# Optimization experiments

Measured on AMD Instinct MI355X. Metric: run time of the kernel, lower is better.

The kernel has to match this reference:

```python
import jax, jax.numpy as jnp
import numpy as np

B, N, D = 4, 1024, 1024
H, DH = 16, 64            # heads, dim_head; inner_dim = H*DH = D
CTX_N, CTX_D = 77, 768    # CLIP text context
FF_IN, FF_HID = 8 * D, 4 * D  # GEGLU: proj to 2*4*D, gate to 4*D
EPS = 1e-5
SCALE = DH ** -0.5
NL = 256                  # 2**8 levels for all quantizers
ZP_QKV = 128.0            # asymmetric 8-bit zero point for q/k/v
ZP_W = 0.0                # always_zero=True for softmax-weight quantizer


def _round_ste(t):
    return t + jax.lax.stop_gradient(jnp.round(t) - t)


def _fake_quant(x, delta, zp):
    xq = jnp.clip(_round_ste(x / delta) + zp, 0.0, NL - 1.0)
    return (xq - zp) * delta


def _ln(x, w, b):
    m = x.mean(-1, keepdims=True)
    v = x.var(-1, keepdims=True)
    return (x - m) * jax.lax.rsqrt(v + EPS) * w + b


def _split_heads(t):  # [b, n, h*d] -> [b, h, n, d]
    b, n, _ = t.shape
    return t.reshape(b, n, H, DH).transpose(0, 2, 1, 3)


def _attn(x, ctx, wq, wk, wv, wo, bo, dq, dk, dv, dw):
    q = _split_heads(x @ wq)
    k = _split_heads(ctx @ wk)
    v = _split_heads(ctx @ wv)
    qq = _fake_quant(q, dq, ZP_QKV)
    kk = _fake_quant(k, dk, ZP_QKV)
    sim = jnp.einsum('bhid,bhjd->bhij', qq, kk) * SCALE
    attn = jax.nn.softmax(sim, axis=-1)
    aw = _fake_quant(attn, dw, ZP_W)
    vv = _fake_quant(v, dv, ZP_QKV)
    out = jnp.einsum('bhij,bhjd->bhid', aw, vv)
    b, _, n, _ = out.shape
    out = out.transpose(0, 2, 1, 3).reshape(b, n, H * DH)
    return out @ wo + bo


def _geglu_ff(x, w1, b1, w2, b2):
    h = x @ w1 + b1
    a, g = jnp.split(h, 2, axis=-1)
    return (a * jax.nn.gelu(g, approximate=False)) @ w2 + b2


def setup_inputs() -> dict:
    key = jax.random.key(0)
    ks = jax.random.split(key, 16)
    w = lambda i, shp, s: jax.random.normal(ks[i], shp, jnp.float32) * s
    sD = D ** -0.5
    sC = CTX_D ** -0.5
    return {
        'x': jax.random.normal(ks[0], (B, N, D), jnp.float32),
        'context': jax.random.normal(ks[1], (B, CTX_N, CTX_D), jnp.float32),
        'norm1_w': jnp.ones((D,), jnp.float32), 'norm1_b': jnp.zeros((D,), jnp.float32),
        'norm2_w': jnp.ones((D,), jnp.float32), 'norm2_b': jnp.zeros((D,), jnp.float32),
        'norm3_w': jnp.ones((D,), jnp.float32), 'norm3_b': jnp.zeros((D,), jnp.float32),
        'a1_wq': w(2, (D, D), sD), 'a1_wk': w(3, (D, D), sD), 'a1_wv': w(4, (D, D), sD),
        'a1_wo': w(5, (D, D), sD), 'a1_bo': jnp.zeros((D,), jnp.float32),
        'a2_wq': w(6, (D, D), sD), 'a2_wk': w(7, (CTX_D, D), sC), 'a2_wv': w(8, (CTX_D, D), sC),
        'a2_wo': w(9, (D, D), sD), 'a2_bo': jnp.zeros((D,), jnp.float32),
        'ff_w1': w(10, (D, FF_IN), sD), 'ff_b1': jnp.zeros((FF_IN,), jnp.float32),
        'ff_w2': w(11, (FF_HID, D), FF_HID ** -0.5), 'ff_b2': jnp.zeros((D,), jnp.float32),
        'd1_q': jnp.asarray(0.02, jnp.float32), 'd1_k': jnp.asarray(0.02, jnp.float32),
        'd1_v': jnp.asarray(0.02, jnp.float32), 'd1_w': jnp.asarray(1.0 / 255.0, jnp.float32),
        'd2_q': jnp.asarray(0.02, jnp.float32), 'd2_k': jnp.asarray(0.02, jnp.float32),
        'd2_v': jnp.asarray(0.02, jnp.float32), 'd2_w': jnp.asarray(1.0 / 255.0, jnp.float32),
    }


def reference(x, context, norm1_w, norm1_b, norm2_w, norm2_b, norm3_w, norm3_b,
              a1_wq, a1_wk, a1_wv, a1_wo, a1_bo,
              a2_wq, a2_wk, a2_wv, a2_wo, a2_bo,
              ff_w1, ff_b1, ff_w2, ff_b2,
              d1_q, d1_k, d1_v, d1_w, d2_q, d2_k, d2_v, d2_w):
    # attn1: quantized self-attention
    x = _attn(_ln(x, norm1_w, norm1_b), _ln(x, norm1_w, norm1_b),
              a1_wq, a1_wk, a1_wv, a1_wo, a1_bo, d1_q, d1_k, d1_v, d1_w) + x
    # attn2: quantized cross-attention with text context
    x = _attn(_ln(x, norm2_w, norm2_b), context,
              a2_wq, a2_wk, a2_wv, a2_wo, a2_bo, d2_q, d2_k, d2_v, d2_w) + x
    # GEGLU feed-forward
    x = _geglu_ff(_ln(x, norm3_w, norm3_b), ff_w1, ff_b1, ff_w2, ff_b2) + x
    return x
```

## Files before the change

kernel.cpp:

```cpp
#include <hip/hip_runtime.h>
#include <math.h>


typedef unsigned short u16;
typedef __attribute__((ext_vector_type(8))) short short8;
typedef __attribute__((ext_vector_type(4))) float f32x4;

__device__ inline float b2f(u16 v) { return __uint_as_float(((unsigned)v) << 16); }
__device__ inline u16 f2b(float f) {
  unsigned u = __float_as_uint(f);
  unsigned r = u + 0x7fffu + ((u >> 16) & 1u);
  return (u16)(r >> 16);
}

__device__ inline float exp2_fast(float x) {
#if __has_builtin(__builtin_amdgcn_exp2f)
  return __builtin_amdgcn_exp2f(x);
#else
  return __expf(x * 0.6931471805599453f);
#endif
}

__device__ inline void glds16(const u16* g, u16* l) {
  __builtin_amdgcn_global_load_lds(
      (const __attribute__((address_space(1))) void*)g,
      (__attribute__((address_space(3))) void*)l, 16, 0, 0);
}

__global__ __launch_bounds__(256) void transpose_k(const float* __restrict__ in,
                                                   u16* __restrict__ out,
                                                   int R, int C) {
  __shared__ float t[32][33];
  int tx = threadIdx.x & 31, ty = threadIdx.x >> 5;
  int c0 = blockIdx.x * 32, r0 = blockIdx.y * 32;
#pragma unroll
  for (int i = 0; i < 32; i += 8)
    t[ty + i][tx] = in[(size_t)(r0 + ty + i) * C + c0 + tx];
  __syncthreads();
#pragma unroll
  for (int i = 0; i < 32; i += 8)
    out[(size_t)(c0 + ty + i) * R + r0 + tx] = f2b(t[tx][ty + i]);
}

struct TrBatch { const float* in[4]; u16* out[4]; int R[4]; };
__global__ __launch_bounds__(256) void transpose4_k(TrBatch a) {
  int z = blockIdx.z;
  const float* in = a.in[z];
  u16* out = a.out[z];
  int R = a.R[z];
  int r0 = blockIdx.y * 32;
  if (r0 >= R) return;
  __shared__ float t[32][33];
  int tx = threadIdx.x & 31, ty = threadIdx.x >> 5;
  int c0 = blockIdx.x * 32;
#pragma unroll
  for (int i = 0; i < 32; i += 8)
    t[ty + i][tx] = in[(size_t)(r0 + ty + i) * 1024 + c0 + tx];
  __syncthreads();
#pragma unroll
  for (int i = 0; i < 32; i += 8)
    out[(size_t)(c0 + ty + i) * R + r0 + tx] = f2b(t[tx][ty + i]);
}

__global__ __launch_bounds__(256) void tr16_k(const u16* __restrict__ in,
                                              u16* __restrict__ out, int NK,
                                              int NKP) {
  __shared__ u16 t[32][33];
  int tx = threadIdx.x & 31, ty = threadIdx.x >> 5;
  int n0 = blockIdx.x * 32, c0 = blockIdx.y * 32, b = blockIdx.z;
  const u16* ib = in + (size_t)b * NK * 1024;
  u16* ob = out + (size_t)b * 1024 * NKP;
#pragma unroll
  for (int i = 0; i < 32; i += 8) {
    int n = n0 + ty + i;
    n = n < NK ? n : NK - 1;
    t[ty + i][tx] = ib[(size_t)n * 1024 + c0 + tx];
  }
  __syncthreads();
#pragma unroll
  for (int i = 0; i < 32; i += 8)
    ob[(size_t)(c0 + ty + i) * NKP + n0 + tx] = t[tx][ty + i];
}

__global__ __launch_bounds__(256) void cast_k(const float* __restrict__ in,
                                              u16* __restrict__ out) {
  int i = (blockIdx.x * 256 + threadIdx.x) * 4;
  float4 v = *(const float4*)(in + i);
  out[i + 0] = f2b(v.x);
  out[i + 1] = f2b(v.y);
  out[i + 2] = f2b(v.z);
  out[i + 3] = f2b(v.w);
}

__global__ __launch_bounds__(256) void ln_k(const float* __restrict__ X,
                                            const float* __restrict__ W,
                                            const float* __restrict__ Bi,
                                            u16* __restrict__ Out) {
  const int row = blockIdx.x, tid = threadIdx.x;
  float4 x = *(const float4*)(X + (size_t)row * 1024 + tid * 4);
  float s = x.x + x.y + x.z + x.w;
  float s2 = x.x * x.x + x.y * x.y + x.z * x.z + x.w * x.w;
#pragma unroll
  for (int off = 32; off >= 1; off >>= 1) {
    s += __shfl_down(s, off);
    s2 += __shfl_down(s2, off);
  }
  __shared__ float red[8];
  int wave = tid >> 6, lane = tid & 63;
  if (lane == 0) { red[wave] = s; red[4 + wave] = s2; }
  __syncthreads();
  s = red[0] + red[1] + red[2] + red[3];
  s2 = red[4] + red[5] + red[6] + red[7];
  float mean = s * 0.0009765625f;
  float var = s2 * 0.0009765625f - mean * mean;
  float rs = rsqrtf(var + 1e-5f);
  float4 w = *(const float4*)(W + tid * 4);
  float4 b = *(const float4*)(Bi + tid * 4);
  u16* orow = Out + (size_t)row * 1024 + tid * 4;
  orow[0] = f2b((x.x - mean) * rs * w.x + b.x);
  orow[1] = f2b((x.y - mean) * rs * w.y + b.y);
  orow[2] = f2b((x.z - mean) * rs * w.z + b.z);
  orow[3] = f2b((x.w - mean) * rs * w.w + b.w);
}

template <int EPI, int TM>
__global__ __launch_bounds__(256, 2) void gemm_bt(
    const u16* __restrict__ A, int lda, const u16* __restrict__ Bt, int ldb,
    void* __restrict__ Cp, int ldc, const float* __restrict__ bias,
    const float* __restrict__ res, int ldr, const float* __restrict__ dp,
    const float* __restrict__ dp2, const float* __restrict__ dp3,
    size_t segsz, int M, int N, int K) {
  __shared__ __align__(16) u16 As[TM * 64];
  __shared__ __align__(16) u16 Bs[128 * 64];
  const int tid = threadIdx.x;
  const int lane = tid & 63, wave = tid >> 6;
  const int qd = lane >> 4, cl = lane & 15;
  const int wm = (wave & 1) * (TM / 2), wn = (wave >> 1) << 6;
  const int m0 = blockIdx.x * TM, n0 = blockIdx.y * 128;

  f32x4 acc[TM / 32][4];
  const f32x4 zero = {0.f, 0.f, 0.f, 0.f};
#pragma unroll
  for (int i = 0; i < TM / 32; i++)
#pragma unroll
    for (int j = 0; j < 4; j++) acc[i][j] = zero;

  for (int k0 = 0; k0 < K; k0 += 64) {
    __syncthreads();
#pragma unroll
    for (int it = 0; it < TM / 32; ++it) {
      int ch = it * 256 + tid;
      int r = ch >> 3, cc = (ch & 7) << 3;
      int gr = m0 + r;
      gr = gr < M ? gr : M - 1;
      glds16(A + (size_t)gr * lda + k0 + cc, As + ch * 8);
    }
#pragma unroll
    for (int it = 0; it < 4; ++it) {
      int ch = it * 256 + tid;
      int r = ch >> 3, cc = (ch & 7) << 3;
      glds16(Bt + (size_t)(n0 + r) * ldb + k0 + cc, Bs + ch * 8);
    }
    __syncthreads();
#pragma unroll
    for (int ks = 0; ks < 64; ks += 32) {
      short8 af[TM / 32], bf[4];
#pragma unroll
      for (int t = 0; t < TM / 32; t++)
        af[t] = *(const short8*)(As + (wm + t * 16 + cl) * 64 + ks + qd * 8);
#pragma unroll
      for (int t = 0; t < 4; t++)
        bf[t] = *(const short8*)(Bs + (wn + t * 16 + cl) * 64 + ks + qd * 8);
#pragma unroll
      for (int mt = 0; mt < TM / 32; mt++)
#pragma unroll
        for (int nt = 0; nt < 4; nt++)
          acc[mt][nt] = __builtin_amdgcn_mfma_f32_16x16x32_bf16(
              af[mt], bf[nt], acc[mt][nt], 0, 0, 0);
    }
  }

  float dscale = 1.f;
  u16* qbase = (u16*)Cp;
  if constexpr (EPI == 0) dscale = 1.0f / dp[0];
  if constexpr (EPI == 2) {
    int seg = n0 >> 10;
    const float* ds = (seg == 0) ? dp : ((seg == 1) ? dp2 : dp3);
    dscale = 1.0f / ds[0];
    qbase = (u16*)Cp + (size_t)seg * segsz;
  }
#pragma unroll
  for (int mt = 0; mt < TM / 32; ++mt) {
#pragma unroll
    for (int r = 0; r < 4; ++r) {
      int row = m0 + wm + mt * 16 + qd * 4 + r;
      if (row >= M) continue;
#pragma unroll
      for (int nt = 0; nt < 4; ++nt) {
        int col = n0 + wn + nt * 16 + cl;
        float v = acc[mt][nt][r];
        if constexpr (EPI == 0) {
          float xq = rintf(v * dscale) + 128.f;
          xq = fminf(fmaxf(xq, 0.f), 255.f);
          qbase[(size_t)row * ldc + col] = f2b(xq - 128.f);
        } else if constexpr (EPI == 2) {
          float xq = rintf(v * dscale) + 128.f;
          xq = fminf(fmaxf(xq, 0.f), 255.f);
          qbase[(size_t)row * ldc + (col & 1023)] = f2b(xq - 128.f);
        } else {
          v += bias[col] + res[(size_t)row * ldr + col];
          ((float*)Cp)[(size_t)row * ldc + col] = v;
        }
      }
    }
  }
}

#define VMW(n) asm volatile("s_waitcnt vmcnt(" #n ")" ::: "memory")
#define LGKM0() asm volatile("s_waitcnt lgkmcnt(0)" ::: "memory")
#define SBAR() __builtin_amdgcn_s_barrier()
#define SCHED0() __builtin_amdgcn_sched_barrier(0)

#define ST_A(P, MH, K0)                                                      \
  do {                                                                       \
    _Pragma("unroll") for (int it = 0; it < 2; ++it) {                       \
      int r_ = (MH) * 128 + it * 64 + sr;                                    \
      glds16(Ag + (size_t)(m0 + r_) * 1024 + (K0) + ((sc ^ (r_ & 7)) << 3),  \
             As + (P) * 16384 + r_ * 64 + (sc << 3));                        \
    }                                                                        \
  } while (0)

#define ST_B(P, BH, K0)                                                      \
  do {                                                                       \
    _Pragma("unroll") for (int it = 0; it < 2; ++it) {                       \
      int r_ = it * 64 + sr;                                                 \
      glds16(W1t + (size_t)((BH) * 4096 + n0 + r_) * 1024 + (K0) +           \
                 ((sc ^ (r_ & 7)) << 3),                                     \
             Bs + (P) * 16384 + ((BH) * 128 + r_) * 64 + (sc << 3));         \
    }                                                                        \
  } while (0)

#define RDA(P, MH)                                                           \
  do {                                                                       \
    _Pragma("unroll") for (int mf = 0; mf < 4; ++mf) {                       \
      int row_ = (MH) * 128 + wr * 64 + mf * 16 + cl;                        \
      _Pragma("unroll") for (int ks = 0; ks < 2; ++ks)                       \
        af[mf * 2 + ks] = *(const short8*)(As + (P) * 16384 + row_ * 64 +    \
                                           (((ks * 4 + qd) ^ (cl & 7)) << 3)); \
    }                                                                        \
  } while (0)

#define RDB(P, NH, DST)                                                      \
  do {                                                                       \
    _Pragma("unroll") for (int nf = 0; nf < 2; ++nf) {                       \
      int j_ = (NH) * 128 + wc * 32 + nf * 16 + cl;                          \
      _Pragma("unroll") for (int ks = 0; ks < 2; ++ks)                       \
        DST[nf * 2 + ks] = *(const short8*)(Bs + (P) * 16384 + j_ * 64 +     \
                                            (((ks * 4 + qd) ^ (cl & 7)) << 3)); \
    }                                                                        \
  } while (0)

#define MFMAQ(MH, NH, BSET)                                                  \
  do {                                                                       \
    _Pragma("unroll") for (int mf = 0; mf < 4; ++mf)                         \
      _Pragma("unroll") for (int nf = 0; nf < 2; ++nf)                       \
        _Pragma("unroll") for (int ks = 0; ks < 2; ++ks)                     \
          acc[(MH) * 4 + mf][(NH) * 2 + nf] =                                \
              __builtin_amdgcn_mfma_f32_16x16x32_bf16(                       \
                  af[mf * 2 + ks], BSET[nf * 2 + ks],                        \
                  acc[(MH) * 4 + mf][(NH) * 2 + nf], 0, 0, 0);               \
  } while (0)

#define KTILE(P, KN, LAST)                                                   \
  do {                                                                       \
                            \
    RDA(P, 0);                                                               \
    RDB(P, 0, bU);                                                           \
    if (!(LAST)) ST_A((P) ^ 1, 0, KN);                                       \
    SBAR();                                                                  \
    LGKM0();                                                                 \
    SCHED0();                                                                \
    __builtin_amdgcn_s_setprio(1);                                           \
    MFMAQ(0, 0, bU);                                                         \
    __builtin_amdgcn_s_setprio(0);                                           \
    SCHED0();                                                                \
    if (LAST) { VMW(0); } else { VMW(2); }                                   \
    SBAR();                                                                  \
                                    \
    RDB(P, 1, bV);                                                           \
    if (!(LAST)) ST_B((P) ^ 1, 0, KN);                                       \
    SBAR();                                                                  \
    LGKM0();                                                                 \
    SCHED0();                                                                \
    __builtin_amdgcn_s_setprio(1);                                           \
    MFMAQ(0, 1, bV);                                                         \
    __builtin_amdgcn_s_setprio(0);                                           \
    SCHED0();                                                                \
    SBAR();                                                                  \
                                    \
    RDA(P, 1);                                                               \
    if (!(LAST)) ST_A((P) ^ 1, 1, KN);                                       \
    SBAR();                                                                  \
    LGKM0();                                                                 \
    SCHED0();                                                                \
    __builtin_amdgcn_s_setprio(1);                                           \
    MFMAQ(1, 1, bV);                                                         \
    __builtin_amdgcn_s_setprio(0);                                           \
    SCHED0();                                                                \
    SBAR();                                                                  \
                                       \
    if (!(LAST)) ST_B((P) ^ 1, 1, KN);                                       \
    SBAR();                                                                  \
    LGKM0();                                                                 \
    SCHED0();                                                                \
    __builtin_amdgcn_s_setprio(1);                                           \
    MFMAQ(1, 0, bU);                                                         \
    __builtin_amdgcn_s_setprio(0);                                           \
    SCHED0();                                                                \
    if (!(LAST)) VMW(4);                                                     \
    SBAR();                                                                  \
  } while (0)

__global__ __launch_bounds__(512, 1) void ff1_geglu8_k(
    const u16* __restrict__ Ag, const u16* __restrict__ W1t,
    const float* __restrict__ b1, u16* __restrict__ gg) {
  __shared__ __align__(16) u16 smem[65536];
  u16* As = smem;
  u16* Bs = smem + 32768;
  const int tid = threadIdx.x;
  const int lane = tid & 63, wave = tid >> 6;
  const int qd = lane >> 4, cl = lane & 15;
  const int wr = wave >> 2, wc = wave & 3;
  const int m0 = blockIdx.x * 256;
  const int n0 = blockIdx.y * 128;
  const int sr = tid >> 3, sc = tid & 7;

  f32x4 acc[8][4];
  const f32x4 zero = {0.f, 0.f, 0.f, 0.f};
#pragma unroll
  for (int i = 0; i < 8; ++i)
#pragma unroll
    for (int j = 0; j < 4; ++j) acc[i][j] = zero;
  short8 af[8], bU[4], bV[4];

  ST_A(0, 0, 0);
  ST_B(0, 0, 0);
  ST_A(0, 1, 0);
  ST_B(0, 1, 0);
  VMW(0);
  SBAR();
  SCHED0();

  int p = 0;
#pragma unroll 1
  for (int t = 0; t < 15; ++t) {
    KTILE(p, (t + 1) * 64, 0);
    p ^= 1;
  }
  KTILE(1, 0, 1);

#pragma unroll
  for (int i = 0; i < 8; ++i) {
    const int row = m0 + (i >> 2) * 128 + wr * 64 + (i & 3) * 16 + qd * 4;
#pragma unroll
    for (int nf = 0; nf < 2; ++nf) {
      const int col = n0 + wc * 32 + nf * 16 + cl;
      const float ba = b1[col];
      const float bg = b1[4096 + col];
#pragma unroll
      for (int r = 0; r < 4; ++r) {
        float a = acc[i][nf][r] + ba;
        float g = acc[i][2 + nf][r] + bg;
        float ge = 0.5f * g * (1.0f + erff(g * 0.70710678118654752f));
        gg[(size_t)(row + r) * 4096 + col] = f2b(a * ge);
      }
    }
  }
}

__global__ __launch_bounds__(256, 4) void attn_k(
    const u16* __restrict__ Q, const u16* __restrict__ Kb,
    const u16* __restrict__ VbT, u16* __restrict__ O,
    const float* dqp, const float* dkp, const float* dvp, const float* dwp,
    int NK, int NKP) {
  __shared__ __align__(16) u16 Ks[64 * 64];
  __shared__ __align__(16) u16 VTs[64 * 64];
  __shared__ __align__(16) u16 Ps[4][16 * 72];
  const int tid = threadIdx.x;
  const int lane = tid & 63, wave = tid >> 6;
  const int qd = lane >> 4, cl = lane & 15;
  const int b = blockIdx.z, h = blockIdx.y, qt = blockIdx.x;
  const float ss2 = dqp[0] * dkp[0] * 0.125f * 1.4426950408889634f;
  const float oscale = dwp[0] * dvp[0];
  const float inv_dw = 1.0f / dwp[0];
  const f32x4 zero = {0.f, 0.f, 0.f, 0.f};

  short8 qf0, qf1;
  {
    const u16* qrow =
        Q + (size_t)(b * 1024 + qt * 64 + wave * 16 + cl) * 1024 + h * 64;
    qf0 = *(const short8*)(qrow + qd * 8);
    qf1 = *(const short8*)(qrow + 32 + qd * 8);
  }

  const u16* kbase = Kb + (size_t)(b * NK) * 1024 + h * 64;
  const u16* vtbase = VbT + ((size_t)b * 1024 + h * 64) * NKP;
  const int r_st = tid >> 3;
  const int c_sw = (((tid & 7) ^ (r_st & 7)) << 3);

  float m_s = -1e30f, l_s = 0.f;
  for (int j0 = 0; j0 < NK; j0 += 64) {
    __syncthreads();
#pragma unroll
    for (int it = 0; it < 2; ++it) {
      int j = j0 + it * 32 + r_st;
      j = j < NK ? j : NK - 1;
      glds16(kbase + (size_t)j * 1024 + c_sw, Ks + (it * 256 + tid) * 8);
    }
    __syncthreads();
    const bool full = (j0 + 64 <= NK);
    float sc[16];
#pragma unroll
    for (int nt = 0; nt < 4; ++nt) {
      const int row = nt * 16 + cl, sw = cl & 7;
      short8 kf0 = *(const short8*)(Ks + row * 64 + ((qd ^ sw) << 3));
      short8 kf1 = *(const short8*)(Ks + row * 64 + (((4 | qd) ^ sw) << 3));
      f32x4 st = zero;
      st = __builtin_amdgcn_mfma_f32_16x16x32_bf16(kf0, qf0, st, 0, 0, 0);
      st = __builtin_amdgcn_mfma_f32_16x16x32_bf16(kf1, qf1, st, 0, 0, 0);
#pragma unroll
      for (int r = 0; r < 4; ++r) {
        int key = j0 + nt * 16 + qd * 4 + r;
        sc[nt * 4 + r] = (full || key < NK) ? st[r] * ss2 : -1e30f;
      }
    }
    float t0 = fmaxf(fmaxf(sc[0], sc[1]), sc[2]);
    float t1 = fmaxf(fmaxf(sc[3], sc[4]), sc[5]);
    float t2 = fmaxf(fmaxf(sc[6], sc[7]), sc[8]);
    float t3 = fmaxf(fmaxf(sc[9], sc[10]), sc[11]);
    float t4 = fmaxf(fmaxf(sc[12], sc[13]), sc[14]);
    float mx = fmaxf(fmaxf(fmaxf(t0, t1), fmaxf(t2, t3)), fmaxf(t4, sc[15]));
    mx = fmaxf(mx, __shfl_xor(mx, 16));
    mx = fmaxf(mx, __shfl_xor(mx, 32));
    float mn = fmaxf(m_s, mx);
    float ss = 0.f;
#pragma unroll
    for (int i = 0; i < 16; ++i) ss += exp2_fast(sc[i] - mn);
    ss += __shfl_xor(ss, 16);
    ss += __shfl_xor(ss, 32);
    l_s = l_s * exp2_fast(m_s - mn) + ss;
    m_s = mn;
  }
  const float mb = m_s + log2f(l_s) - log2f(inv_dw);

  f32x4 oacc[4];
#pragma unroll
  for (int t = 0; t < 4; t++) oacc[t] = zero;

  for (int j0 = 0; j0 < NK; j0 += 64) {
    __syncthreads();
#pragma unroll
    for (int it = 0; it < 2; ++it) {
      int r = it * 32 + r_st;
      int j = j0 + r;
      j = j < NK ? j : NK - 1;
      glds16(kbase + (size_t)j * 1024 + c_sw, Ks + (it * 256 + tid) * 8);
      glds16(vtbase + (size_t)r * NKP + j0 + c_sw, VTs + (it * 256 + tid) * 8);
    }
    __syncthreads();
    const bool full = (j0 + 64 <= NK);
#pragma unroll
    for (int nt = 0; nt < 4; ++nt) {
      const int row = nt * 16 + cl, sw = cl & 7;
      short8 kf0 = *(const short8*)(Ks + row * 64 + ((qd ^ sw) << 3));
      short8 kf1 = *(const short8*)(Ks + row * 64 + (((4 | qd) ^ sw) << 3));
      f32x4 st = zero;
      st = __builtin_amdgcn_mfma_f32_16x16x32_bf16(kf0, qf0, st, 0, 0, 0);
      st = __builtin_amdgcn_mfma_f32_16x16x32_bf16(kf1, qf1, st, 0, 0, 0);
      unsigned a[4];
#pragma unroll
      for (int r = 0; r < 4; ++r) {
        int key = j0 + nt * 16 + qd * 4 + r;
        float aw = 0.f;
        if (full || key < NK) {
          float e = exp2_fast(__builtin_fmaf(st[r], ss2, -mb));
          aw = fminf(rintf(e), 255.f);
        }
        a[r] = __float_as_uint(aw);
      }
      uint2 pv;
      pv.x = (a[0] >> 16) | (a[1] & 0xffff0000u);
      pv.y = (a[2] >> 16) | (a[3] & 0xffff0000u);
      *(uint2*)(&Ps[wave][cl * 72 + nt * 16 + qd * 4]) = pv;
    }
#pragma unroll
    for (int ks = 0; ks < 2; ++ks) {
      short8 pf = *(const short8*)(&Ps[wave][cl * 72 + ks * 32 + qd * 8]);
#pragma unroll
      for (int dt = 0; dt < 4; ++dt) {
        const int vrow = dt * 16 + cl;
        short8 vf = *(const short8*)(VTs + vrow * 64 +
                                     (((ks * 4 + qd) ^ (cl & 7)) << 3));
        oacc[dt] = __builtin_amdgcn_mfma_f32_16x16x32_bf16(pf, vf, oacc[dt],
                                                           0, 0, 0);
      }
    }
  }
#pragma unroll
  for (int dt = 0; dt < 4; ++dt)
#pragma unroll
    for (int r = 0; r < 4; r++) {
      size_t addr =
          (size_t)(b * 1024 + qt * 64 + wave * 16 + qd * 4 + r) * 1024 +
          h * 64 + dt * 16 + cl;
      O[addr] = f2b(oacc[dt][r] * oscale);
    }
}

extern "C" void kernel_launch(void* const* d_in, const int* in_sizes, int n_in,
                              void* d_out, int out_size, void* d_ws,
                              size_t ws_size, hipStream_t stream) {
  (void)in_sizes; (void)n_in; (void)out_size; (void)ws_size;
  const float* x    = (const float*)d_in[0];
  const float* ctx  = (const float*)d_in[1];
  const float* n1w  = (const float*)d_in[2];
  const float* n1b  = (const float*)d_in[3];
  const float* n2w  = (const float*)d_in[4];
  const float* n2b  = (const float*)d_in[5];
  const float* n3w  = (const float*)d_in[6];
  const float* n3b  = (const float*)d_in[7];
  const float* a1wq = (const float*)d_in[8];
  const float* a1wk = (const float*)d_in[9];
  const float* a1wv = (const float*)d_in[10];
  const float* a1wo = (const float*)d_in[11];
  const float* a1bo = (const float*)d_in[12];
  const float* a2wq = (const float*)d_in[13];
  const float* a2wk = (const float*)d_in[14];
  const float* a2wv = (const float*)d_in[15];
  const float* a2wo = (const float*)d_in[16];
  const float* a2bo = (const float*)d_in[17];
  const float* ffw1 = (const float*)d_in[18];
  const float* ffb1 = (const float*)d_in[19];
  const float* ffw2 = (const float*)d_in[20];
  const float* ffb2 = (const float*)d_in[21];
  const float* d1q = (const float*)d_in[22];
  const float* d1k = (const float*)d_in[23];
  const float* d1v = (const float*)d_in[24];
  const float* d1w = (const float*)d_in[25];
  const float* d2q = (const float*)d_in[26];
  const float* d2k = (const float*)d_in[27];
  const float* d2v = (const float*)d_in[28];
  const float* d2w = (const float*)d_in[29];

  char* ws = (char*)d_ws;
  const size_t MB = 1u << 20;
  u16* W    = (u16*)(ws + 0 * MB);
  u16* lnb  = (u16*)(ws + 16 * MB);
  u16* qb   = (u16*)(ws + 24 * MB);
  u16* kb   = (u16*)(ws + 32 * MB);
  u16* vb   = (u16*)(ws + 40 * MB);
  u16* vbT  = (u16*)(ws + 48 * MB);
  u16* ao   = (u16*)(ws + 56 * MB);
  float* x1 = (float*)(ws + 64 * MB);
  u16* k2b  = (u16*)(ws + 32 * MB);
  u16* v2b  = k2b + 308 * 1024;
  u16* vbTc = (u16*)(ws + 34 * MB);
  u16* ctxb = (u16*)(ws + 35 * MB);
  u16* gg   = (u16*)(ws + 24 * MB);

  u16* WT0 = W;
  u16* WT1 = (u16*)(ws + 2 * MB);
  u16* WT2 = (u16*)(ws + 4 * MB);
  u16* WT3 = (u16*)(ws + 6 * MB);
  u16* WT3c = WT2 + 1024 * 768;

  dim3 T256(256);
  {
    TrBatch tb;
    tb.in[0] = a1wq; tb.out[0] = WT0; tb.R[0] = 1024;
    tb.in[1] = a1wk; tb.out[1] = WT1; tb.R[1] = 1024;
    tb.in[2] = a1wv; tb.out[2] = WT2; tb.R[2] = 1024;
    tb.in[3] = a1wo; tb.out[3] = WT3; tb.R[3] = 1024;
    transpose4_k<<<dim3(32, 32, 4), T256, 0, stream>>>(tb);
  }
  ln_k<<<4096, T256, 0, stream>>>(x, n1w, n1b, lnb);
  gemm_bt<2, 128><<<dim3(32, 24), T256, 0, stream>>>(
      lnb, 1024, WT0, 1024, qb, 1024, nullptr, nullptr, 0, d1q, d1k, d1v,
      (size_t)4096 * 1024, 4096, 3072, 1024);
  tr16_k<<<dim3(32, 32, 4), T256, 0, stream>>>(vb, vbT, 1024, 1024);
  attn_k<<<dim3(16, 16, 4), T256, 0, stream>>>(qb, kb, vbT, ao, d1q, d1k, d1v,
                                               d1w, 1024, 1024);
  gemm_bt<1, 64><<<dim3(64, 8), T256, 0, stream>>>(
      ao, 1024, WT3, 1024, x1, 1024, a1bo, x, 1024, nullptr, nullptr, nullptr,
      0, 4096, 1024, 1024);
  {
    TrBatch tb;
    tb.in[0] = a2wq; tb.out[0] = WT0; tb.R[0] = 1024;
    tb.in[1] = a2wo; tb.out[1] = WT1; tb.R[1] = 1024;
    tb.in[2] = a2wk; tb.out[2] = WT2;  tb.R[2] = 768;
    tb.in[3] = a2wv; tb.out[3] = WT3c; tb.R[3] = 768;
    transpose4_k<<<dim3(32, 32, 4), T256, 0, stream>>>(tb);
  }
  ln_k<<<4096, T256, 0, stream>>>(x1, n2w, n2b, lnb);
  cast_k<<<231, T256, 0, stream>>>(ctx, ctxb);
  gemm_bt<0, 64><<<dim3(64, 8), T256, 0, stream>>>(
      lnb, 1024, WT0, 1024, qb, 1024, nullptr, nullptr, 0, d2q, nullptr,
      nullptr, 0, 4096, 1024, 1024);
  gemm_bt<2, 64><<<dim3(5, 16), T256, 0, stream>>>(
      ctxb, 768, WT2, 768, k2b, 1024, nullptr, nullptr, 0, d2k, d2v, nullptr,
      (size_t)308 * 1024, 308, 2048, 768);
  tr16_k<<<dim3(3, 32, 4), T256, 0, stream>>>(v2b, vbTc, 77, 128);
  attn_k<<<dim3(16, 16, 4), T256, 0, stream>>>(qb, k2b, vbTc, ao, d2q, d2k,
                                               d2v, d2w, 77, 128);
  gemm_bt<1, 64><<<dim3(64, 8), T256, 0, stream>>>(
      ao, 1024, WT1, 1024, x1, 1024, a2bo, x1, 1024, nullptr, nullptr, nullptr,
      0, 4096, 1024, 1024);
  transpose_k<<<dim3(256, 32), T256, 0, stream>>>(ffw1, W, 1024, 8192);
  ln_k<<<4096, T256, 0, stream>>>(x1, n3w, n3b, lnb);
  ff1_geglu8_k<<<dim3(16, 32), dim3(512), 0, stream>>>(lnb, W, ffb1, gg);
  transpose_k<<<dim3(32, 128), T256, 0, stream>>>(ffw2, W, 4096, 1024);
  gemm_bt<1, 64><<<dim3(64, 8), T256, 0, stream>>>(
      gg, 4096, W, 4096, d_out, 1024, ffb2, x1, 1024, nullptr, nullptr,
      nullptr, 0, 4096, 1024, 4096);
}
```

Baseline: 546.0 us.

## Split-K the FF2 GEMM with atomic accumulation into a zeroed output

Replaces the final FF2 GEMM (M=4096, N=1024, K=4096) with a new split-K kernel. It uses 128x128 tiles and K split in two, giving 512 blocks, and accumulates partial sums into the output with float atomicAdd. Only the first K-slice adds bias and residual, and a zero kernel clears the output first. This is meant to raise parallelism and occupancy over the previous 64x8 grid. In exchange it costs an extra zeroing pass, atomic traffic on 4M floats, and a simpler single-buffered mainloop with no LDS swizzle, which may have bank conflicts.

```diff
diff --git a/kernel.cpp b/kernel.cpp
--- a/kernel.cpp
+++ b/kernel.cpp
@@ -90,6 +90,11 @@
   out[i + 1] = f2b(v.y);
   out[i + 2] = f2b(v.z);
   out[i + 3] = f2b(v.w);
+}
+
+__global__ __launch_bounds__(256) void zero_k(float4* __restrict__ out) {
+  float4 z = {0.f, 0.f, 0.f, 0.f};
+  out[blockIdx.x * 256 + threadIdx.x] = z;
 }
 
 __global__ __launch_bounds__(256) void ln_k(const float* __restrict__ X,
@@ -211,6 +216,76 @@
           v += bias[col] + res[(size_t)row * ldr + col];
           ((float*)Cp)[(size_t)row * ldc + col] = v;
         }
+      }
+    }
+  }
+}
+
+__global__ __launch_bounds__(256, 2) void gemm_bt_sk(
+    const u16* __restrict__ A, int lda, const u16* __restrict__ Bt, int ldb,
+    float* __restrict__ C, int ldc, const float* __restrict__ bias,
+    const float* __restrict__ res, int ldr, int M, int KH) {
+  __shared__ __align__(16) u16 As[128 * 64];
+  __shared__ __align__(16) u16 Bs[128 * 64];
+  const int tid = threadIdx.x;
+  const int lane = tid & 63, wave = tid >> 6;
+  const int qd = lane >> 4, cl = lane & 15;
+  const int wm = (wave & 1) * 64, wn = (wave >> 1) << 6;
+  const int m0 = blockIdx.x * 128, n0 = blockIdx.y * 128;
+  const int kz = blockIdx.z;
+  const int kbeg = kz * KH, kend = kbeg + KH;
+
+  f32x4 acc[4][4];
+  const f32x4 zero = {0.f, 0.f, 0.f, 0.f};
+#pragma unroll
+  for (int i = 0; i < 4; i++)
+#pragma unroll
+    for (int j = 0; j < 4; j++) acc[i][j] = zero;
+
+  for (int k0 = kbeg; k0 < kend; k0 += 64) {
+    __syncthreads();
+#pragma unroll
+    for (int it = 0; it < 4; ++it) {
+      int ch = it * 256 + tid;
+      int r = ch >> 3, cc = (ch & 7) << 3;
+      glds16(A + (size_t)(m0 + r) * lda + k0 + cc, As + ch * 8);
+    }
+#pragma unroll
+    for (int it = 0; it < 4; ++it) {
+      int ch = it * 256 + tid;
+      int r = ch >> 3, cc = (ch & 7) << 3;
+      glds16(Bt + (size_t)(n0 + r) * ldb + k0 + cc, Bs + ch * 8);
+    }
+    __syncthreads();
+#pragma unroll
+    for (int ks = 0; ks < 64; ks += 32) {
+      short8 af[4], bf[4];
+#pragma unroll
+      for (int t = 0; t < 4; t++)
+        af[t] = *(const short8*)(As + (wm + t * 16 + cl) * 64 + ks + qd * 8);
+#pragma unroll
+      for (int t = 0; t < 4; t++)
+        bf[t] = *(const short8*)(Bs + (wn + t * 16 + cl) * 64 + ks + qd * 8);
+#pragma unroll
+      for (int mt = 0; mt < 4; mt++)
+#pragma unroll
+        for (int nt = 0; nt < 4; nt++)
+          acc[mt][nt] = __builtin_amdgcn_mfma_f32_16x16x32_bf16(
+              af[mt], bf[nt], acc[mt][nt], 0, 0, 0);
+    }
+  }
+
+#pragma unroll
+  for (int mt = 0; mt < 4; ++mt) {
+#pragma unroll
+    for (int r = 0; r < 4; ++r) {
+      int row = m0 + wm + mt * 16 + qd * 4 + r;
+#pragma unroll
+      for (int nt = 0; nt < 4; ++nt) {
+        int col = n0 + wn + nt * 16 + cl;
+        float v = acc[mt][nt][r];
+        if (kz == 0) v += bias[col] + res[(size_t)row * ldr + col];
+        atomicAdd(&C[(size_t)row * ldc + col], v);
       }
     }
   }
@@ -619,7 +694,7 @@
   ln_k<<<4096, T256, 0, stream>>>(x1, n3w, n3b, lnb);
   ff1_geglu8_k<<<dim3(16, 32), dim3(512), 0, stream>>>(lnb, W, ffb1, gg);
   transpose_k<<<dim3(32, 128), T256, 0, stream>>>(ffw2, W, 4096, 1024);
-  gemm_bt<1, 64><<<dim3(64, 8), T256, 0, stream>>>(
-      gg, 4096, W, 4096, d_out, 1024, ffb2, x1, 1024, nullptr, nullptr,
-      nullptr, 0, 4096, 1024, 4096);
-}
+  zero_k<<<4096, T256, 0, stream>>>((float4*)d_out);
+  gemm_bt_sk<<<dim3(32, 8, 2), T256, 0, stream>>>(
+      gg, 4096, W, 4096, (float*)d_out, 1024, ffb2, x1, 1024, 4096, 2048);
+}
```

Measured after the change: 557.0 us. +2.0%, slower.
